# Kernel optimization log

Measured on AMD Instinct MI355X. Metric: run time of the kernel, lower is better.

## Reference

```python
import jax, jax.numpy as jnp
import numpy as np

GRAY_W = jnp.array([0.2989, 0.587, 0.114], dtype=jnp.float32)  # torchvision rgb_to_grayscale


def bilinear_sample(img, sx, sy):
    """img: [..., H, W]; sx, sy: [Ho, Wo] source pixel coords; zero padding (grid_sample bilinear)."""
    H, W = img.shape[-2], img.shape[-1]
    x0 = jnp.floor(sx)
    y0 = jnp.floor(sy)
    wx1 = sx - x0
    wy1 = sy - y0
    wx0 = 1.0 - wx1
    wy0 = 1.0 - wy1

    def gather(xi, yi):
        valid = (xi >= 0) & (xi <= W - 1) & (yi >= 0) & (yi <= H - 1)
        xc = jnp.clip(xi, 0, W - 1).astype(jnp.int32)
        yc = jnp.clip(yi, 0, H - 1).astype(jnp.int32)
        return img[..., yc, xc] * valid.astype(img.dtype)

    return (gather(x0, y0) * (wy0 * wx0) + gather(x0 + 1.0, y0) * (wy0 * wx1)
            + gather(x0, y0 + 1.0) * (wy1 * wx0) + gather(x0 + 1.0, y0 + 1.0) * (wy1 * wx1))


def forward(adv_patch, lab_batch, img_size):
    B, L = lab_batch.shape[0], lab_batch.shape[1]
    N, S = B * L, img_size
    key = jax.random.key(42)
    kb, kc, ks, kn, ka, ksc, kp = jax.random.split(key, 7)

    # Resize (bilinear, half-pixel centers). All N expanded copies are identical at this
    # point, so resize + color-jitter once on the single patch, then broadcast (same math).
    p = jax.image.resize(adv_patch, (3, S, S), method="bilinear")

    # ColorJitter: one factor per transform per call, applied to the whole batch.
    b = jax.random.uniform(kb, (), minval=0.8, maxval=1.1)
    c = jax.random.uniform(kc, (), minval=0.8, maxval=1.1)
    s = jax.random.uniform(ks, (), minval=0.8, maxval=1.1)
    p = p * b                                                    # brightness
    p = c * p + (1.0 - c) * jnp.einsum('chw,c->hw', p, GRAY_W).mean()   # contrast
    p = s * p + (1.0 - s) * jnp.einsum('chw,c->hw', p, GRAY_W)[None]    # saturation

    # Uniform noise in [-1,1] * noise_factor, per element of the full [N,3,S,S] batch.
    batch = p[None] + 0.15 * jax.random.uniform(kn, (N, 3, S, S), minval=-1.0, maxval=1.0)

    # RandomAffine(degrees=(-45,45), scale=(0.1,0.16)): rotation+scale about image
    # center, one sample per call; inverse map, shared [S,S] grid for all N images.
    theta = jnp.deg2rad(jax.random.uniform(ka, (), minval=-45.0, maxval=45.0))
    sc = jax.random.uniform(ksc, (), minval=0.1, maxval=0.16)
    ctr = (S - 1) / 2.0
    xs = jnp.arange(S, dtype=jnp.float32) - ctr
    dy, dx = jnp.meshgrid(xs, xs, indexing='ij')
    cos_t, sin_t = jnp.cos(theta), jnp.sin(theta)
    sx = (cos_t * dx + sin_t * dy) / sc + ctr
    sy = (-sin_t * dx + cos_t * dy) / sc + ctr
    batch = bilinear_sample(batch, sx, sy)

    # RandomPerspective(distortion_scale=0.6, p=1.0): corners pulled inward by random
    # integer offsets in [0, 0.6*half]; solve homography T with T(endpoint)=startpoint
    # (output->source map), shared for the whole batch.
    dmax = int(0.6 * (S // 2))
    r = jax.random.randint(kp, (8,), 0, dmax + 1).astype(jnp.float32)
    w = jnp.float32(S - 1)
    end = jnp.stack([jnp.stack([r[0], r[1]]),
                     jnp.stack([w - r[2], r[3]]),
                     jnp.stack([w - r[4], w - r[5]]),
                     jnp.stack([r[6], w - r[7]])])  # [4,2] endpoints (tl,tr,br,bl)
    start = jnp.array([[0.0, 0.0], [1.0, 0.0], [1.0, 1.0], [0.0, 1.0]], jnp.float32) * w
    ex, ey = end[:, 0], end[:, 1]
    px, py = start[:, 0], start[:, 1]
    z, o = jnp.zeros(4, jnp.float32), jnp.ones(4, jnp.float32)
    A = jnp.concatenate([
        jnp.stack([ex, ey, o, z, z, z, -px * ex, -px * ey], axis=1),
        jnp.stack([z, z, z, ex, ey, o, -py * ex, -py * ey], axis=1)], axis=0)  # [8,8]
    rhs = jnp.concatenate([px, py])
    h = jnp.linalg.solve(A, rhs)
    xo = jnp.arange(S, dtype=jnp.float32) + 0.5  # torchvision perspective grid offset
    yo_g, xo_g = jnp.meshgrid(xo, xo, indexing='ij')
    den = h[6] * xo_g + h[7] * yo_g + 1.0
    psx = (h[0] * xo_g + h[1] * yo_g + h[2]) / den - 0.5
    psy = (h[3] * xo_g + h[4] * yo_g + h[5]) / den - 0.5
    batch = bilinear_sample(batch, psx, psy)

    return jnp.clip(batch, 0.0, 0.99).reshape(B, L, 3, S, S)


def setup_inputs() -> dict:
    key = jax.random.key(0)
    k1, k2 = jax.random.split(key)
    return {
        "adv_patch": jax.random.uniform(k1, (3, 300, 300), dtype=jnp.float32),
        "lab_batch": jax.random.normal(k2, (8, 14, 5), dtype=jnp.float32),
        "img_size": 416,
    }


def reference(adv_patch, lab_batch, img_size):
    return forward(adv_patch, lab_batch, img_size)
```

## Files before the change

### kernel.cpp

```cpp
#include <hip/hip_runtime.h>
#include <cstdint>
#include <cstring>
#include <cmath>

__host__ __device__ static inline uint32_t rotl32(uint32_t x, int r) {
  return (x << r) | (x >> (32 - r));
}

__host__ __device__ static inline void tf2x32(uint32_t k0, uint32_t k1,
                                              uint32_t c0, uint32_t c1,
                                              uint32_t& o0, uint32_t& o1) {
  const uint32_t ks2 = 0x1BD11BDAu ^ k0 ^ k1;
  uint32_t x0 = c0 + k0;
  uint32_t x1 = c1 + k1;
#define TF_QR(r) { x0 += x1; x1 = rotl32(x1, (r)); x1 ^= x0; }
  TF_QR(13) TF_QR(15) TF_QR(26) TF_QR(6)
  x0 += k1;  x1 += ks2 + 1u;
  TF_QR(17) TF_QR(29) TF_QR(16) TF_QR(24)
  x0 += ks2; x1 += k0 + 2u;
  TF_QR(13) TF_QR(15) TF_QR(26) TF_QR(6)
  x0 += k0;  x1 += k1 + 3u;
  TF_QR(17) TF_QR(29) TF_QR(16) TF_QR(24)
  x0 += k1;  x1 += ks2 + 4u;
  TF_QR(13) TF_QR(15) TF_QR(26) TF_QR(6)
  x0 += ks2; x1 += k0 + 5u;
#undef TF_QR
  o0 = x0; o1 = x1;
}

__host__ __device__ static inline uint32_t tf_bits32(uint32_t k0, uint32_t k1, uint32_t i) {
  uint32_t a, b;
  tf2x32(k0, k1, 0u, i, a, b);
  return a ^ b;
}

__device__ static inline float noise_from_bits(uint32_t bits) {
  uint32_t fb = (bits >> 9) | 0x3f800000u;
  float f = __uint_as_float(fb) - 1.0f;
  float v = f * 2.0f - 1.0f;
  v = fmaxf(-1.0f, v);
  return 0.15f * v;
}

__device__ static inline void zero_role(int g, int Gtot, int N, int S, int X8,
                                        int blo, int bhi, float4* __restrict__ out,
                                        float h0, float h1, float h2, float h3,
                                        float h4, float h5, float h6, float h7) {
  if (g >= Gtot) return;
  int x8 = g % X8;
  int t2 = g / X8;
  int y  = t2 % S;
  int n  = t2 / S;
  float yo  = (float)y + 0.5f;
  float xo0 = (float)(x8 * 8) + 0.5f;
  float xo7 = xo0 + 7.0f;
  float den0 = h6 * xo0 + h7 * yo + 1.0f;
  float den7 = h6 * xo7 + h7 * yo + 1.0f;
  float psx0 = (h0 * xo0 + h1 * yo + h2) / den0 - 0.5f;
  float psy0 = (h3 * xo0 + h4 * yo + h5) / den0 - 0.5f;
  float psx7 = (h0 * xo7 + h1 * yo + h2) / den7 - 0.5f;
  float psy7 = (h3 * xo7 + h4 * yo + h5) / den7 - 0.5f;
  float lox = fminf(psx0, psx7), hix = fmaxf(psx0, psx7);
  float loy = fminf(psy0, psy7), hiy = fmaxf(psy0, psy7);
  float bl = (float)blo - 1.5f, bh = (float)bhi + 1.5f;
  bool exterior = (den0 > 0.0f) && (den7 > 0.0f) &&
                  (hix < bl || lox > bh || hiy < bl || loy > bh);
  if (!exterior) return;
  int X4 = X8 * 2;
  size_t obase = ((size_t)(n * 3) * S + y) * X4 + x8 * 2;
  size_t ostride = (size_t)S * X4;
  float4 z = make_float4(0.f, 0.f, 0.f, 0.f);
  out[obase]                = z;
  out[obase + 1]            = z;
  out[obase + ostride]      = z;
  out[obase + ostride + 1]  = z;
  out[obase + 2 * ostride]     = z;
  out[obase + 2 * ostride + 1] = z;
}

__global__ void __launch_bounds__(256)
k_resize_z(const float* __restrict__ src, float4* __restrict__ p1,
           double* __restrict__ part, float bmul, int S, int inS, int SS, int nbA,
           int zstart, int Gtot, int N, int X8, int blo, int bhi,
           float4* __restrict__ out,
           float h0, float h1, float h2, float h3, float h4, float h5, float h6, float h7) {
  if ((int)blockIdx.x >= nbA) {
    int g = zstart + ((int)blockIdx.x - nbA) * 256 + (int)threadIdx.x;
    zero_role(g, Gtot, N, S, X8, blo, bhi, out, h0, h1, h2, h3, h4, h5, h6, h7);
    return;
  }
  __shared__ double sh[256];
  int t = blockIdx.x * 256 + threadIdx.x;
  double g = 0.0;
  if (t < SS) {
    int y = t / S, x = t - y * S;
    float fs = (float)inS / (float)S;
    float fy = ((float)y + 0.5f) * fs - 0.5f;
    float fx = ((float)x + 0.5f) * fs - 0.5f;
    float y0f = floorf(fy), x0f = floorf(fx);
    float ty = fy - y0f, tx = fx - x0f;
    int y0 = (int)y0f, x0 = (int)x0f;
    int y1 = y0 + 1, x1 = x0 + 1;
    y0 = min(max(y0, 0), inS - 1); y1 = min(max(y1, 0), inS - 1);
    x0 = min(max(x0, 0), inS - 1); x1 = min(max(x1, 0), inS - 1);
    float w00 = (1.f - ty) * (1.f - tx), w01 = (1.f - ty) * tx;
    float w10 = ty * (1.f - tx),         w11 = ty * tx;
    float rgb[3];
    for (int c = 0; c < 3; ++c) {
      const float* pc = src + (size_t)c * inS * inS;
      float v = pc[y0 * inS + x0] * w00 + pc[y0 * inS + x1] * w01 +
                pc[y1 * inS + x0] * w10 + pc[y1 * inS + x1] * w11;
      v *= bmul;
      rgb[c] = v;
    }
    p1[t] = make_float4(rgb[0], rgb[1], rgb[2], 0.0f);
    g = (double)(0.2989f * rgb[0] + 0.587f * rgb[1] + 0.114f * rgb[2]);
  }
  sh[threadIdx.x] = g;
  __syncthreads();
  for (int s2 = 128; s2 > 0; s2 >>= 1) {
    if (threadIdx.x < s2) sh[threadIdx.x] += sh[threadIdx.x + s2];
    __syncthreads();
  }
  if (threadIdx.x == 0) part[blockIdx.x] = sh[0];
}

__global__ void __launch_bounds__(256)
k_combined(const float4* __restrict__ p1, float* __restrict__ b1,
           const double* __restrict__ part, int nb,
           float cc, float ssat,
           uint32_t kn0, uint32_t kn1, int S, int SS, int blo, int bhi, int bw, int bwp,
           float cos_t, float sin_t, float sc, float ctr, int N, int X8,
           int NB1, int NTOT, int zstart, int Gtot,
           float4* __restrict__ out,
           float h0, float h1, float h2, float h3, float h4, float h5, float h6, float h7) {
  int b = blockIdx.x;
  long long tt = (long long)b * NB1;
  int h_before = (int)(tt / NTOT);
  int h_incl   = (int)((tt + NB1) / NTOT);
  bool is_hash = (h_incl > h_before);

  if (!is_hash) {
    int zb = b - h_before;
    int g = zstart + zb * 256 + (int)threadIdx.x;
    zero_role(g, Gtot, N, S, X8, blo, bhi, out, h0, h1, h2, h3, h4, h5, h6, h7);
    return;
  }

  __shared__ double sh[256];
  double a = 0.0;
  for (int i = threadIdx.x; i < nb; i += 256) a += part[i];
  sh[threadIdx.x] = a;
  __syncthreads();
  for (int s2 = 128; s2 > 0; s2 >>= 1) {
    if (threadIdx.x < s2) sh[threadIdx.x] += sh[threadIdx.x + s2];
    __syncthreads();
  }
  float m = (float)(sh[0] / (double)SS);

  int idx = h_before * 256 + threadIdx.x;
  if (idx >= bw * bw * N) return;
  int px = idx % bw;
  int t2 = idx / bw;
  int py = t2 % bw;
  int n  = t2 / bw;

  int xt = blo + px, yt = blo + py;
  float dx = (float)xt - ctr, dy = (float)yt - ctr;
  float sx = (cos_t * dx + sin_t * dy) / sc + ctr;
  float sy = (-sin_t * dx + cos_t * dy) / sc + ctr;
  float x0f = floorf(sx), y0f = floorf(sy);
  float wx1 = sx - x0f, wy1 = sy - y0f;
  float wx0 = 1.f - wx1, wy0 = 1.f - wy1;
  float Wm1 = (float)(S - 1);
  float xtf[4] = {x0f, x0f + 1.f, x0f, x0f + 1.f};
  float ytf[4] = {y0f, y0f, y0f + 1.f, y0f + 1.f};
  float wt[4]  = {wy0 * wx0, wy0 * wx1, wy1 * wx0, wy1 * wx1};
  float acc[3] = {0.f, 0.f, 0.f};
  uint32_t nbase = (uint32_t)(n * 3) * (uint32_t)SS;
  float omc = 1.0f - cc, oms = 1.0f - ssat;
#pragma unroll
  for (int u = 0; u < 4; ++u) {
    bool valid = (xtf[u] >= 0.f) && (xtf[u] <= Wm1) && (ytf[u] >= 0.f) && (ytf[u] <= Wm1);
    if (!valid) continue;
    int ix = (int)xtf[u], iy = (int)ytf[u];
    int sp = iy * S + ix;
    float4 p = p1[sp];
    float r2 = cc * p.x + omc * m;
    float g2 = cc * p.y + omc * m;
    float b2 = cc * p.z + omc * m;
    float gray = 0.2989f * r2 + 0.587f * g2 + 0.114f * b2;
    float pfv[3];
    pfv[0] = ssat * r2 + oms * gray;
    pfv[1] = ssat * g2 + oms * gray;
    pfv[2] = ssat * b2 + oms * gray;
    uint32_t idx0 = nbase + (uint32_t)sp;
#pragma unroll
    for (int c = 0; c < 3; ++c) {
      uint32_t bits = tf_bits32(kn0, kn1, idx0 + (uint32_t)(c * SS));
      acc[c] += wt[u] * (pfv[c] + noise_from_bits(bits));
    }
  }
#pragma unroll
  for (int c = 0; c < 3; ++c)
    b1[(((size_t)n * 3 + c) * bw + py) * bwp + px] = acc[c];
}

__global__ void __launch_bounds__(256)
k_out_in_z(const float* __restrict__ b1, float4* __restrict__ out,
           int S, int X8, int blo, int bhi, int bw, int bwp,
           int ylo, int rows, int glo, int gcnt, int totalInt, int nbInt,
           int zstart, int Gtot, int N,
           float h0, float h1, float h2, float h3, float h4, float h5, float h6, float h7) {
  if ((int)blockIdx.x >= nbInt) {
    int g = zstart + ((int)blockIdx.x - nbInt) * 256 + (int)threadIdx.x;
    zero_role(g, Gtot, N, S, X8, blo, bhi, out, h0, h1, h2, h3, h4, h5, h6, h7);
    return;
  }
  int tid = blockIdx.x * 256 + threadIdx.x;
  if (tid >= totalInt) return;
  int x8 = glo + tid % gcnt;
  int t2 = tid / gcnt;
  int y  = ylo + t2 % rows;
  int n  = t2 / rows;

  int X4 = X8 * 2;
  float yo  = (float)y + 0.5f;
  float xo0 = (float)(x8 * 8) + 0.5f;
  float xo7 = xo0 + 7.0f;
  float den0 = h6 * xo0 + h7 * yo + 1.0f;
  float den7 = h6 * xo7 + h7 * yo + 1.0f;
  float psx0 = (h0 * xo0 + h1 * yo + h2) / den0 - 0.5f;
  float psy0 = (h3 * xo0 + h4 * yo + h5) / den0 - 0.5f;
  float psx7 = (h0 * xo7 + h1 * yo + h2) / den7 - 0.5f;
  float psy7 = (h3 * xo7 + h4 * yo + h5) / den7 - 0.5f;
  float lox = fminf(psx0, psx7), hix = fmaxf(psx0, psx7);
  float loy = fminf(psy0, psy7), hiy = fmaxf(psy0, psy7);
  float bl = (float)blo - 1.5f, bh = (float)bhi + 1.5f;
  bool exterior = (den0 > 0.0f) && (den7 > 0.0f) &&
                  (hix < bl || lox > bh || hiy < bl || loy > bh);
  if (exterior) return;

  float acc[3][8];
#pragma unroll
  for (int c = 0; c < 3; ++c)
#pragma unroll
    for (int j = 0; j < 8; ++j) acc[c][j] = 0.f;

  float Wm1 = (float)(S - 1);
#pragma unroll
  for (int j = 0; j < 8; ++j) {
    float xo = (float)(x8 * 8 + j) + 0.5f;
    float den = h6 * xo + h7 * yo + 1.0f;
    float psx = (h0 * xo + h1 * yo + h2) / den - 0.5f;
    float psy = (h3 * xo + h4 * yo + h5) / den - 0.5f;
    float x0f = floorf(psx), y0f = floorf(psy);
    float wx1 = psx - x0f, wy1 = psy - y0f;
    float wx0 = 1.f - wx1, wy0 = 1.f - wy1;
    float xtf[4] = {x0f, x0f + 1.f, x0f, x0f + 1.f};
    float ytf[4] = {y0f, y0f, y0f + 1.f, y0f + 1.f};
    float wt[4]  = {wy0 * wx0, wy0 * wx1, wy1 * wx0, wy1 * wx1};
#pragma unroll
    for (int u = 0; u < 4; ++u) {
      bool valid = (xtf[u] >= 0.f) && (xtf[u] <= Wm1) && (ytf[u] >= 0.f) && (ytf[u] <= Wm1);
      if (!valid) continue;
      int ix = (int)xtf[u] - blo;
      int iy = (int)ytf[u] - blo;
      if (ix < 0 || ix >= bw || iy < 0 || iy >= bw) continue;
#pragma unroll
      for (int c = 0; c < 3; ++c)
        acc[c][j] += wt[u] * b1[(((size_t)n * 3 + c) * bw + iy) * bwp + ix];
    }
  }

  size_t obase = ((size_t)(n * 3) * S + y) * X4 + x8 * 2;
  size_t ostride = (size_t)S * X4;
#pragma unroll
  for (int c = 0; c < 3; ++c) {
    float4 v0, v1;
    v0.x = fminf(fmaxf(acc[c][0], 0.0f), 0.99f);
    v0.y = fminf(fmaxf(acc[c][1], 0.0f), 0.99f);
    v0.z = fminf(fmaxf(acc[c][2], 0.0f), 0.99f);
    v0.w = fminf(fmaxf(acc[c][3], 0.0f), 0.99f);
    v1.x = fminf(fmaxf(acc[c][4], 0.0f), 0.99f);
    v1.y = fminf(fmaxf(acc[c][5], 0.0f), 0.99f);
    v1.z = fminf(fmaxf(acc[c][6], 0.0f), 0.99f);
    v1.w = fminf(fmaxf(acc[c][7], 0.0f), 0.99f);
    out[obase + (size_t)c * ostride]     = v0;
    out[obase + (size_t)c * ostride + 1] = v1;
  }
}

static float bits_to_u01_host(uint32_t bits) {
  uint32_t fb = (bits >> 9) | 0x3f800000u;
  float f;
  std::memcpy(&f, &fb, 4);
  return f - 1.0f;
}

static float host_uniform(uint32_t k0, uint32_t k1, float mn, float mx) {
  uint32_t bits = tf_bits32(k0, k1, 0u);
  float f = bits_to_u01_host(bits);
  float d = mx - mn;
  float t = f * d;
  float v = t + mn;
  return v < mn ? mn : v;
}

static void solve8(float A[8][8], float b[8], float x[8]) {
  for (int k = 0; k < 8; ++k) {
    int piv = k;
    float amax = fabsf(A[k][k]);
    for (int i = k + 1; i < 8; ++i) {
      float v = fabsf(A[i][k]);
      if (v > amax) { amax = v; piv = i; }
    }
    if (piv != k) {
      for (int j = 0; j < 8; ++j) { float t = A[k][j]; A[k][j] = A[piv][j]; A[piv][j] = t; }
      float t = b[k]; b[k] = b[piv]; b[piv] = t;
    }
    for (int i = k + 1; i < 8; ++i) {
      float l = A[i][k] / A[k][k];
      A[i][k] = l;
      for (int j = k + 1; j < 8; ++j) A[i][j] -= l * A[k][j];
      b[i] -= l * b[k];
    }
  }
  for (int i = 7; i >= 0; --i) {
    float s = b[i];
    for (int j = i + 1; j < 8; ++j) s -= A[i][j] * x[j];
    x[i] = s / A[i][i];
  }
}

extern "C" void kernel_launch(void* const* d_in, const int* in_sizes, int n_in,
                              void* d_out, int out_size, void* d_ws, size_t ws_size,
                              hipStream_t stream) {
  const float* adv = (const float*)d_in[0];
  float* out = (float*)d_out;

  int inS = (int)llround(sqrt((double)in_sizes[0] / 3.0));
  int N   = in_sizes[1] / 5;
  if (N <= 0) N = 112;
  int S   = (int)llround(sqrt((double)out_size / (3.0 * N)));
  int SS  = S * S;

  uint32_t K[7][2];
  for (int i = 0; i < 7; ++i)
    tf2x32(0u, 42u, 0u, (uint32_t)i, K[i][0], K[i][1]);

  float bmul = host_uniform(K[0][0], K[0][1], 0.8f, 1.1f);
  float cc   = host_uniform(K[1][0], K[1][1], 0.8f, 1.1f);
  float ssat = host_uniform(K[2][0], K[2][1], 0.8f, 1.1f);
  float adeg = host_uniform(K[4][0], K[4][1], -45.f, 45.f);
  float theta = adeg * (float)(M_PI / 180.0);
  float sc   = host_uniform(K[5][0], K[5][1], 0.1f, 0.16f);
  float cos_t = cosf(theta), sin_t = sinf(theta);

  int dmax = (int)(0.6 * (double)(S / 2));
  uint32_t span = (uint32_t)(dmax + 1);
  uint32_t mult = ((65536u % span) * (65536u % span)) % span;
  uint32_t kp1[2], kp2[2];
  tf2x32(K[6][0], K[6][1], 0u, 0u, kp1[0], kp1[1]);
  tf2x32(K[6][0], K[6][1], 0u, 1u, kp2[0], kp2[1]);
  float r[8];
  for (int i = 0; i < 8; ++i) {
    uint32_t hi = tf_bits32(kp1[0], kp1[1], (uint32_t)i);
    uint32_t lo = tf_bits32(kp2[0], kp2[1], (uint32_t)i);
    uint32_t v = ((hi % span) * mult + (lo % span)) % span;
    r[i] = (float)v;
  }

  float w = (float)(S - 1);
  float ex[4] = {r[0], w - r[2], w - r[4], r[6]};
  float ey[4] = {r[1], r[3], w - r[5], w - r[7]};
  float px4[4] = {0.f, w, w, 0.f};
  float py4[4] = {0.f, 0.f, w, w};
  float A[8][8];
  float rhs[8];
  for (int i = 0; i < 4; ++i) {
    A[i][0] = ex[i]; A[i][1] = ey[i]; A[i][2] = 1.f;
    A[i][3] = 0.f;   A[i][4] = 0.f;   A[i][5] = 0.f;
    A[i][6] = -px4[i] * ex[i]; A[i][7] = -px4[i] * ey[i];
    rhs[i] = px4[i];
    A[4 + i][0] = 0.f; A[4 + i][1] = 0.f; A[4 + i][2] = 0.f;
    A[4 + i][3] = ex[i]; A[4 + i][4] = ey[i]; A[4 + i][5] = 1.f;
    A[4 + i][6] = -py4[i] * ex[i]; A[4 + i][7] = -py4[i] * ey[i];
    rhs[4 + i] = py4[i];
  }
  float h[8];
  solve8(A, rhs, h);

  float ctr = (float)(S - 1) * 0.5f;
  float a_half = (ctr + 2.0f) * sc;
  float bbh = a_half * (fabsf(cos_t) + fabsf(sin_t)) + 3.0f;
  int blo = (int)floorf(ctr - bbh); if (blo < 0) blo = 0;
  int bhi = (int)ceilf(ctr + bbh);  if (bhi > S - 1) bhi = S - 1;
  int bw = bhi - blo + 1;
  int bwp = (bw + 15) & ~15;

  int X8 = S / 8;
  int ylo = S, yhi = -1, glo = X8, ghi = -1;
  {
    double H0 = h[0], H1 = h[1], H2 = h[2], H3 = h[3], H4 = h[4], H5 = h[5], H6 = h[6], H7 = h[7];
    double bl = (double)blo - 3.0, bh = (double)bhi + 3.0;
    for (int y = 0; y < S; ++y) {
      double yo = y + 0.5;
      for (int g = 0; g < X8; ++g) {
        double xo0 = g * 8 + 0.5, xo7 = xo0 + 7.0;
        double den0 = H6 * xo0 + H7 * yo + 1.0;
        double den7 = H6 * xo7 + H7 * yo + 1.0;
        bool ext;
        if (den0 > 0.0 && den7 > 0.0) {
          double psx0 = (H0 * xo0 + H1 * yo + H2) / den0 - 0.5;
          double psy0 = (H3 * xo0 + H4 * yo + H5) / den0 - 0.5;
          double psx7 = (H0 * xo7 + H1 * yo + H2) / den7 - 0.5;
          double psy7 = (H3 * xo7 + H4 * yo + H5) / den7 - 0.5;
          double lox = fmin(psx0, psx7), hix = fmax(psx0, psx7);
          double loy = fmin(psy0, psy7), hiy = fmax(psy0, psy7);
          ext = (hix < bl || lox > bh || hiy < bl || loy > bh);
        } else {
          ext = false;
        }
        if (!ext) {
          if (y < ylo) ylo = y;
          if (y > yhi) yhi = y;
          if (g < glo) glo = g;
          if (g > ghi) ghi = g;
        }
      }
    }
  }
  int rows = (yhi >= ylo) ? (yhi - ylo + 1) : 0;
  int gcnt = (ghi >= glo) ? (ghi - glo + 1) : 0;

  size_t psize = (size_t)SS * sizeof(float4);
  float4* p1   = (float4*)d_ws;
  double* part = (double*)((char*)d_ws + psize);
  float*  b1   = (float*)((char*)d_ws + psize + 8192);

  int nbA = (SS + 255) / 256;

  int Gtot = N * S * X8;
  int NZ   = (Gtot + 255) / 256;
  int NB1  = (bw * bw * N + 255) / 256;
  int ZB   = (int)((long long)NZ * 42 / 100);
  int ZA   = (NZ - ZB) / 2;
  int ZC   = NZ - ZB - ZA;
  int zA0  = 0;
  int zB0  = ZA * 256;
  int zC0  = (ZA + ZB) * 256;

  k_resize_z<<<nbA + ZA, 256, 0, stream>>>(
      adv, p1, part, bmul, S, inS, SS, nbA,
      zA0, Gtot, N, X8, blo, bhi, (float4*)out,
      h[0], h[1], h[2], h[3], h[4], h[5], h[6], h[7]);

  int NTOT = NB1 + ZB;
  k_combined<<<NTOT, 256, 0, stream>>>(
      p1, b1, part, nbA, cc, ssat,
      K[3][0], K[3][1], S, SS, blo, bhi, bw, bwp,
      cos_t, sin_t, sc, ctr, N, X8, NB1, NTOT, zB0, Gtot, (float4*)out,
      h[0], h[1], h[2], h[3], h[4], h[5], h[6], h[7]);

  int totalInt = N * rows * gcnt;
  int nbInt = (totalInt + 255) / 256;
  if (totalInt <= 0) nbInt = 0;
  k_out_in_z<<<nbInt + ZC, 256, 0, stream>>>(
      b1, (float4*)out, S, X8, blo, bhi, bw, bwp,
      ylo, rows, glo, gcnt, totalInt, nbInt,
      zC0, Gtot, N,
      h[0], h[1], h[2], h[3], h[4], h[5], h[6], h[7]);
}
```

Before: 74.79 us.

## Fold contrast mean term algebraically to merge three kernels into two

Contrast and saturation are factored so the global-mean contribution becomes a per-pixel weight sum times a constant. That term is applied in the final warp kernel after it reduces the partial sums. This lets the resize+mean reduction, the rotation/noise stage and all zero-fill blocks run in one launch, recomputing the resize directly from the input patch instead of going through a float4 intermediate. The intermediate buffer becomes float4 interleaved (rgb plus accumulated weight). The cost is extra resize gathers per rotation tap and a small reduction repeated in every final-stage block.

```diff
diff --git a/kernel.cpp b/kernel.cpp
--- a/kernel.cpp
+++ b/kernel.cpp
@@ -40,6 +40,28 @@
   float v = f * 2.0f - 1.0f;
   v = fmaxf(-1.0f, v);
   return 0.15f * v;
+}
+
+__device__ static inline void resize_rgb(const float* __restrict__ adv, int inS, int S,
+                                         int x, int y, float bmul, float rgb[3]) {
+  float fs = (float)inS / (float)S;
+  float fy = ((float)y + 0.5f) * fs - 0.5f;
+  float fx = ((float)x + 0.5f) * fs - 0.5f;
+  float y0f = floorf(fy), x0f = floorf(fx);
+  float ty = fy - y0f, tx = fx - x0f;
+  int y0 = (int)y0f, x0 = (int)x0f;
+  int y1 = y0 + 1, x1 = x0 + 1;
+  y0 = min(max(y0, 0), inS - 1); y1 = min(max(y1, 0), inS - 1);
+  x0 = min(max(x0, 0), inS - 1); x1 = min(max(x1, 0), inS - 1);
+  float w00 = (1.f - ty) * (1.f - tx), w01 = (1.f - ty) * tx;
+  float w10 = ty * (1.f - tx),         w11 = ty * tx;
+#pragma unroll
+  for (int c = 0; c < 3; ++c) {
+    const float* pc = adv + (size_t)c * inS * inS;
+    float v = pc[y0 * inS + x0] * w00 + pc[y0 * inS + x1] * w01 +
+              pc[y1 * inS + x0] * w10 + pc[y1 * inS + x1] * w11;
+    rgb[c] = v * bmul;
+  }
 }
 
 __device__ static inline void zero_role(int g, int Gtot, int N, int S, int X8,
@@ -79,84 +101,49 @@
 }
 
 __global__ void __launch_bounds__(256)
-k_resize_z(const float* __restrict__ src, float4* __restrict__ p1,
-           double* __restrict__ part, float bmul, int S, int inS, int SS, int nbA,
-           int zstart, int Gtot, int N, int X8, int blo, int bhi,
-           float4* __restrict__ out,
-           float h0, float h1, float h2, float h3, float h4, float h5, float h6, float h7) {
-  if ((int)blockIdx.x >= nbA) {
-    int g = zstart + ((int)blockIdx.x - nbA) * 256 + (int)threadIdx.x;
+k_fused(const float* __restrict__ adv, float4* __restrict__ b1,
+        double* __restrict__ part, int nbRes,
+        float bmul, float cc, float ssat,
+        uint32_t kn0, uint32_t kn1, int S, int inS, int SS,
+        int blo, int bhi, int bw, int bwp,
+        float cos_t, float sin_t, float sc, float ctr, int N, int X8,
+        int NB1, int NTOT2, int Gtot,
+        float4* __restrict__ out,
+        float h0, float h1, float h2, float h3, float h4, float h5, float h6, float h7) {
+  int b = blockIdx.x;
+
+  if (b < nbRes) {
+    __shared__ double sh[256];
+    int t = b * 256 + threadIdx.x;
+    double g = 0.0;
+    if (t < SS) {
+      int y = t / S, x = t - y * S;
+      float rgb[3];
+      resize_rgb(adv, inS, S, x, y, bmul, rgb);
+      g = (double)(0.2989f * rgb[0] + 0.587f * rgb[1] + 0.114f * rgb[2]);
+    }
+    sh[threadIdx.x] = g;
+    __syncthreads();
+    for (int s2 = 128; s2 > 0; s2 >>= 1) {
+      if (threadIdx.x < s2) sh[threadIdx.x] += sh[threadIdx.x + s2];
+      __syncthreads();
+    }
+    if (threadIdx.x == 0) part[b] = sh[0];
+    return;
+  }
+
+  int b2 = b - nbRes;
+  long long tt = (long long)b2 * NB1;
+  int h_before = (int)(tt / NTOT2);
+  int h_incl   = (int)((tt + NB1) / NTOT2);
+  bool is_hash = (h_incl > h_before);
+
+  if (!is_hash) {
+    int zb = b2 - h_before;
+    int g = zb * 256 + (int)threadIdx.x;
     zero_role(g, Gtot, N, S, X8, blo, bhi, out, h0, h1, h2, h3, h4, h5, h6, h7);
     return;
   }
-  __shared__ double sh[256];
-  int t = blockIdx.x * 256 + threadIdx.x;
-  double g = 0.0;
-  if (t < SS) {
-    int y = t / S, x = t - y * S;
-    float fs = (float)inS / (float)S;
-    float fy = ((float)y + 0.5f) * fs - 0.5f;
-    float fx = ((float)x + 0.5f) * fs - 0.5f;
-    float y0f = floorf(fy), x0f = floorf(fx);
-    float ty = fy - y0f, tx = fx - x0f;
-    int y0 = (int)y0f, x0 = (int)x0f;
-    int y1 = y0 + 1, x1 = x0 + 1;
-    y0 = min(max(y0, 0), inS - 1); y1 = min(max(y1, 0), inS - 1);
-    x0 = min(max(x0, 0), inS - 1); x1 = min(max(x1, 0), inS - 1);
-    float w00 = (1.f - ty) * (1.f - tx), w01 = (1.f - ty) * tx;
-    float w10 = ty * (1.f - tx),         w11 = ty * tx;
-    float rgb[3];
-    for (int c = 0; c < 3; ++c) {
-      const float* pc = src + (size_t)c * inS * inS;
-      float v = pc[y0 * inS + x0] * w00 + pc[y0 * inS + x1] * w01 +
-                pc[y1 * inS + x0] * w10 + pc[y1 * inS + x1] * w11;
-      v *= bmul;
-      rgb[c] = v;
-    }
-    p1[t] = make_float4(rgb[0], rgb[1], rgb[2], 0.0f);
-    g = (double)(0.2989f * rgb[0] + 0.587f * rgb[1] + 0.114f * rgb[2]);
-  }
-  sh[threadIdx.x] = g;
-  __syncthreads();
-  for (int s2 = 128; s2 > 0; s2 >>= 1) {
-    if (threadIdx.x < s2) sh[threadIdx.x] += sh[threadIdx.x + s2];
-    __syncthreads();
-  }
-  if (threadIdx.x == 0) part[blockIdx.x] = sh[0];
-}
-
-__global__ void __launch_bounds__(256)
-k_combined(const float4* __restrict__ p1, float* __restrict__ b1,
-           const double* __restrict__ part, int nb,
-           float cc, float ssat,
-           uint32_t kn0, uint32_t kn1, int S, int SS, int blo, int bhi, int bw, int bwp,
-           float cos_t, float sin_t, float sc, float ctr, int N, int X8,
-           int NB1, int NTOT, int zstart, int Gtot,
-           float4* __restrict__ out,
-           float h0, float h1, float h2, float h3, float h4, float h5, float h6, float h7) {
-  int b = blockIdx.x;
-  long long tt = (long long)b * NB1;
-  int h_before = (int)(tt / NTOT);
-  int h_incl   = (int)((tt + NB1) / NTOT);
-  bool is_hash = (h_incl > h_before);
-
-  if (!is_hash) {
-    int zb = b - h_before;
-    int g = zstart + zb * 256 + (int)threadIdx.x;
-    zero_role(g, Gtot, N, S, X8, blo, bhi, out, h0, h1, h2, h3, h4, h5, h6, h7);
-    return;
-  }
-
-  __shared__ double sh[256];
-  double a = 0.0;
-  for (int i = threadIdx.x; i < nb; i += 256) a += part[i];
-  sh[threadIdx.x] = a;
-  __syncthreads();
-  for (int s2 = 128; s2 > 0; s2 >>= 1) {
-    if (threadIdx.x < s2) sh[threadIdx.x] += sh[threadIdx.x + s2];
-    __syncthreads();
-  }
-  float m = (float)(sh[0] / (double)SS);
 
   int idx = h_before * 256 + threadIdx.x;
   if (idx >= bw * bw * N) return;
@@ -177,46 +164,48 @@
   float ytf[4] = {y0f, y0f, y0f + 1.f, y0f + 1.f};
   float wt[4]  = {wy0 * wx0, wy0 * wx1, wy1 * wx0, wy1 * wx1};
   float acc[3] = {0.f, 0.f, 0.f};
+  float accW = 0.f;
   uint32_t nbase = (uint32_t)(n * 3) * (uint32_t)SS;
-  float omc = 1.0f - cc, oms = 1.0f - ssat;
+  float oms = 1.0f - ssat;
 #pragma unroll
   for (int u = 0; u < 4; ++u) {
     bool valid = (xtf[u] >= 0.f) && (xtf[u] <= Wm1) && (ytf[u] >= 0.f) && (ytf[u] <= Wm1);
     if (!valid) continue;
     int ix = (int)xtf[u], iy = (int)ytf[u];
     int sp = iy * S + ix;
-    float4 p = p1[sp];
-    float r2 = cc * p.x + omc * m;
-    float g2 = cc * p.y + omc * m;
-    float b2 = cc * p.z + omc * m;
-    float gray = 0.2989f * r2 + 0.587f * g2 + 0.114f * b2;
-    float pfv[3];
-    pfv[0] = ssat * r2 + oms * gray;
-    pfv[1] = ssat * g2 + oms * gray;
-    pfv[2] = ssat * b2 + oms * gray;
+    float p[3];
+    resize_rgb(adv, inS, S, ix, iy, bmul, p);
+    float gray_p = 0.2989f * p[0] + 0.587f * p[1] + 0.114f * p[2];
     uint32_t idx0 = nbase + (uint32_t)sp;
 #pragma unroll
     for (int c = 0; c < 3; ++c) {
+      float colored = cc * (ssat * p[c] + oms * gray_p);
       uint32_t bits = tf_bits32(kn0, kn1, idx0 + (uint32_t)(c * SS));
-      acc[c] += wt[u] * (pfv[c] + noise_from_bits(bits));
-    }
-  }
-#pragma unroll
-  for (int c = 0; c < 3; ++c)
-    b1[(((size_t)n * 3 + c) * bw + py) * bwp + px] = acc[c];
+      acc[c] += wt[u] * (colored + noise_from_bits(bits));
+    }
+    accW += wt[u];
+  }
+  b1[((size_t)n * bw + py) * bwp + px] = make_float4(acc[0], acc[1], acc[2], accW);
 }
 
 __global__ void __launch_bounds__(256)
-k_out_in_z(const float* __restrict__ b1, float4* __restrict__ out,
-           int S, int X8, int blo, int bhi, int bw, int bwp,
-           int ylo, int rows, int glo, int gcnt, int totalInt, int nbInt,
-           int zstart, int Gtot, int N,
-           float h0, float h1, float h2, float h3, float h4, float h5, float h6, float h7) {
-  if ((int)blockIdx.x >= nbInt) {
-    int g = zstart + ((int)blockIdx.x - nbInt) * 256 + (int)threadIdx.x;
-    zero_role(g, Gtot, N, S, X8, blo, bhi, out, h0, h1, h2, h3, h4, h5, h6, h7);
-    return;
-  }
+k_out_in2(const float4* __restrict__ b1, float4* __restrict__ out,
+          const double* __restrict__ part, int nbRes, float Km,
+          int S, int SS, int X8, int blo, int bhi, int bw, int bwp,
+          int ylo, int rows, int glo, int gcnt, int totalInt,
+          float h0, float h1, float h2, float h3, float h4, float h5, float h6, float h7) {
+  __shared__ double sh[256];
+  double a = 0.0;
+  for (int i = threadIdx.x; i < nbRes; i += 256) a += part[i];
+  sh[threadIdx.x] = a;
+  __syncthreads();
+  for (int s2 = 128; s2 > 0; s2 >>= 1) {
+    if (threadIdx.x < s2) sh[threadIdx.x] += sh[threadIdx.x + s2];
+    __syncthreads();
+  }
+  float m = (float)(sh[0] / (double)SS);
+  float Kmm = Km * m;
+
   int tid = blockIdx.x * 256 + threadIdx.x;
   if (tid >= totalInt) return;
   int x8 = glo + tid % gcnt;
@@ -259,7 +248,7 @@
     float wx0 = 1.f - wx1, wy0 = 1.f - wy1;
     float xtf[4] = {x0f, x0f + 1.f, x0f, x0f + 1.f};
     float ytf[4] = {y0f, y0f, y0f + 1.f, y0f + 1.f};
-    float wt[4]  = {wy0 * wx0, wy0 * wx1, wy1 * wx0, wy1 * wx1};
+    float wtp[4] = {wy0 * wx0, wy0 * wx1, wy1 * wx0, wy1 * wx1};
 #pragma unroll
     for (int u = 0; u < 4; ++u) {
       bool valid = (xtf[u] >= 0.f) && (xtf[u] <= Wm1) && (ytf[u] >= 0.f) && (ytf[u] <= Wm1);
@@ -267,9 +256,11 @@
       int ix = (int)xtf[u] - blo;
       int iy = (int)ytf[u] - blo;
       if (ix < 0 || ix >= bw || iy < 0 || iy >= bw) continue;
-#pragma unroll
-      for (int c = 0; c < 3; ++c)
-        acc[c][j] += wt[u] * b1[(((size_t)n * 3 + c) * bw + iy) * bwp + ix];
+      float4 v = b1[((size_t)n * bw + iy) * bwp + ix];
+      float mterm = Kmm * v.w;
+      acc[0][j] += wtp[u] * (v.x + mterm);
+      acc[1][j] += wtp[u] * (v.y + mterm);
+      acc[2][j] += wtp[u] * (v.z + mterm);
     }
   }
 
@@ -356,6 +347,10 @@
   float theta = adeg * (float)(M_PI / 180.0);
   float sc   = host_uniform(K[5][0], K[5][1], 0.1f, 0.16f);
   float cos_t = cosf(theta), sin_t = sinf(theta);
+
+  float omc = 1.0f - cc, oms = 1.0f - ssat;
+  float wsum = 0.2989f + 0.587f + 0.114f;
+  float Km = omc * (ssat + oms * wsum);
 
   int dmax = (int)(0.6 * (double)(S / 2));
   uint32_t span = (uint32_t)(dmax + 1);
@@ -434,41 +429,27 @@
   int rows = (yhi >= ylo) ? (yhi - ylo + 1) : 0;
   int gcnt = (ghi >= glo) ? (ghi - glo + 1) : 0;
 
-  size_t psize = (size_t)SS * sizeof(float4);
-  float4* p1   = (float4*)d_ws;
-  double* part = (double*)((char*)d_ws + psize);
-  float*  b1   = (float*)((char*)d_ws + psize + 8192);
-
-  int nbA = (SS + 255) / 256;
-
-  int Gtot = N * S * X8;
-  int NZ   = (Gtot + 255) / 256;
-  int NB1  = (bw * bw * N + 255) / 256;
-  int ZB   = (int)((long long)NZ * 42 / 100);
-  int ZA   = (NZ - ZB) / 2;
-  int ZC   = NZ - ZB - ZA;
-  int zA0  = 0;
-  int zB0  = ZA * 256;
-  int zC0  = (ZA + ZB) * 256;
-
-  k_resize_z<<<nbA + ZA, 256, 0, stream>>>(
-      adv, p1, part, bmul, S, inS, SS, nbA,
-      zA0, Gtot, N, X8, blo, bhi, (float4*)out,
+  double* part = (double*)d_ws;
+  float4* b1   = (float4*)((char*)d_ws + 8192);
+
+  int nbRes = (SS + 255) / 256;
+  int Gtot  = N * S * X8;
+  int NZ    = (Gtot + 255) / 256;
+  int NB1   = (bw * bw * N + 255) / 256;
+  int NTOT2 = NB1 + NZ;
+
+  k_fused<<<nbRes + NTOT2, 256, 0, stream>>>(
+      adv, b1, part, nbRes, bmul, cc, ssat,
+      K[3][0], K[3][1], S, inS, SS, blo, bhi, bw, bwp,
+      cos_t, sin_t, sc, ctr, N, X8, NB1, NTOT2, Gtot, (float4*)out,
       h[0], h[1], h[2], h[3], h[4], h[5], h[6], h[7]);
 
-  int NTOT = NB1 + ZB;
-  k_combined<<<NTOT, 256, 0, stream>>>(
-      p1, b1, part, nbA, cc, ssat,
-      K[3][0], K[3][1], S, SS, blo, bhi, bw, bwp,
-      cos_t, sin_t, sc, ctr, N, X8, NB1, NTOT, zB0, Gtot, (float4*)out,
-      h[0], h[1], h[2], h[3], h[4], h[5], h[6], h[7]);
-
   int totalInt = N * rows * gcnt;
-  int nbInt = (totalInt + 255) / 256;
-  if (totalInt <= 0) nbInt = 0;
-  k_out_in_z<<<nbInt + ZC, 256, 0, stream>>>(
-      b1, (float4*)out, S, X8, blo, bhi, bw, bwp,
-      ylo, rows, glo, gcnt, totalInt, nbInt,
-      zC0, Gtot, N,
-      h[0], h[1], h[2], h[3], h[4], h[5], h[6], h[7]);
-}
+  if (totalInt > 0) {
+    k_out_in2<<<(totalInt + 255) / 256, 256, 0, stream>>>(
+        b1, (float4*)out, part, nbRes, Km,
+        S, SS, X8, blo, bhi, bw, bwp,
+        ylo, rows, glo, gcnt, totalInt,
+        h[0], h[1], h[2], h[3], h[4], h[5], h[6], h[7]);
+  }
+}
```

Result: slower. 86.61 us (+15.8%).
